# Optimization experiments

Measured on AMD Instinct MI355X. Metric: run time of the kernel, lower is better.

## Reference

```python
import jax, jax.numpy as jnp
import numpy as np

MARGIN = 0.9
WIN = 3
SIGMA = 1.5    # kornia ssim default gaussian sigma
PAD = (WIN - 1) // 2


def _gauss2d(win, sigma):
    x = np.arange(win, dtype=np.float64) - (win - 1) / 2.0
    g = np.exp(-(x ** 2) / (2.0 * sigma ** 2))
    g = g / g.sum()
    return jnp.asarray(np.outer(g, g), dtype=jnp.float32)

_KERN = _gauss2d(WIN, SIGMA)[None, None]


def _blur(z):
    # kornia filter2d: reflect padding + gaussian window, 'same' output
    zp = jnp.pad(z, ((0, 0), (0, 0), (PAD, PAD), (PAD, PAD)), mode='reflect')
    return jax.lax.conv_general_dilated(zp, _KERN.astype(z.dtype), (1, 1), 'VALID')


def setup_inputs() -> dict:
    key = jax.random.key(0)
    kernels = jax.random.normal(key, (128, 128, 3, 3), dtype=jnp.float32)
    return {"kernels": kernels}


def reference(kernels):
    C_in, C_out, h, w = kernels.shape
    flat = kernels.reshape(C_in * C_out, h, w)

    # pair indices (constants) -- replicate torch flatten/repeat_interleave order exactly
    bi, bj = np.triu_indices(C_out, k=1)          # P_per_ch pairs
    P = bi.shape[0]
    offs = np.arange(C_in) * C_out
    i_idx = (bi[:, None] + offs[None, :]).ravel() # [P, C_in] row-major flatten
    j_idx = (bj[:, None] + offs[None, :]).ravel()
    ch_id = jnp.asarray(np.repeat(np.arange(C_in), P), dtype=jnp.int32)

    # dynamic range (torch uses .item() -> detached)
    rng = jax.lax.stop_gradient(flat.max() - flat.min())
    rng = jnp.where(rng == 0, jnp.asarray(1.0, flat.dtype), rng)
    C1 = (0.01 * rng) ** 2
    C2 = (0.03 * rng) ** 2

    x = flat[i_idx][:, None]  # [P_total,1,h,w]
    y = flat[j_idx][:, None]

    mu1, mu2 = _blur(x), _blur(y)
    mu1_sq, mu2_sq, mu12 = mu1 * mu1, mu2 * mu2, mu1 * mu2
    s1 = _blur(x * x) - mu1_sq
    s2 = _blur(y * y) - mu2_sq
    s12 = _blur(x * y) - mu12
    ssim_map = ((2.0 * mu12 + C1) * (2.0 * s12 + C2)) / (
        (mu1_sq + mu2_sq + C1) * (s1 + s2 + C2))
    ssim_pair = ssim_map.mean(axis=(1, 2, 3))           # [P_total]

    hinge = jax.nn.relu(ssim_pair - MARGIN)
    pos = (hinge > 0).astype(flat.dtype)
    sums = jax.ops.segment_sum(hinge, ch_id, num_segments=C_in)
    counts = jax.ops.segment_sum(pos, ch_id, num_segments=C_in)
    layer_loss = (sums / jnp.maximum(counts, 1.0)).mean()
    return layer_loss  # total / n_layers with a single layer
```

## Files before the change

kernel.cpp:

```cpp
#include <hip/hip_runtime.h>
#include <math.h>

#define CIN   128
#define COUT  128
#define NMAPS (CIN*COUT)
#define PPC   8128
#define F32S  27
#define F64S  24
#define LCAP  (1u<<21)
#define BPC   8


__device__ inline void decode_pair(int p, int& a, int& b) {
    int a0 = (int)((255.0f - sqrtf((float)(65025 - 8 * p))) * 0.5f);
    if (a0 < 0) a0 = 0;
    if (a0 > 126) a0 = 126;
    while ((a0 + 1) * (255 - (a0 + 1)) / 2 <= p) ++a0;
    while (a0 * (255 - a0) / 2 > p) --a0;
    a = a0;
    b = a0 + 1 + (p - a0 * (255 - a0) / 2);
}

__device__ inline void blur3f(const float* X, float* O, float g0, float g1) {
    float h0 = 2.0f * g0;
    float T[9];
#pragma unroll
    for (int c = 0; c < 3; ++c) {
        float x0 = X[c], x1 = X[3 + c], x2 = X[6 + c];
        T[c]     = g1 * x0 + h0 * x1;
        T[3 + c] = g0 * (x0 + x2) + g1 * x1;
        T[6 + c] = h0 * x1 + g1 * x2;
    }
#pragma unroll
    for (int r = 0; r < 3; ++r) {
        float t0 = T[3 * r], t1 = T[3 * r + 1], t2 = T[3 * r + 2];
        O[3 * r]     = g1 * t0 + h0 * t1;
        O[3 * r + 1] = g0 * (t0 + t2) + g1 * t1;
        O[3 * r + 2] = h0 * t1 + g1 * t2;
    }
}

__device__ inline void blur3d(const double* X, double* O, double g0, double g1) {
    double h0 = 2.0 * g0;
    double T[9];
#pragma unroll
    for (int c = 0; c < 3; ++c) {
        double x0 = X[c], x1 = X[3 + c], x2 = X[6 + c];
        T[c]     = g1 * x0 + h0 * x1;
        T[3 + c] = g0 * (x0 + x2) + g1 * x1;
        T[6 + c] = h0 * x1 + g1 * x2;
    }
#pragma unroll
    for (int r = 0; r < 3; ++r) {
        double t0 = T[3 * r], t1 = T[3 * r + 1], t2 = T[3 * r + 2];
        O[3 * r]     = g1 * t0 + h0 * t1;
        O[3 * r + 1] = g0 * (t0 + t2) + g1 * t1;
        O[3 * r + 2] = h0 * t1 + g1 * t2;
    }
}


__global__ __launch_bounds__(256) void k_pre(const float* __restrict__ in,
                                             float* __restrict__ pre32,
                                             double* __restrict__ pre64,
                                             float* __restrict__ pbmin,
                                             float* __restrict__ pbmax,
                                             float* __restrict__ segsum,
                                             float* __restrict__ segcnt,
                                             unsigned* __restrict__ listc,
                                             float g0f, float g1f,
                                             double g0, double g1) {
    __shared__ float stg[2304];
    int tid = threadIdx.x;
    int base = blockIdx.x * 2304;
    for (int i = tid; i < 2304; i += 256) stg[i] = in[base + i];
    __syncthreads();

    float xf[9];
    float lmin = 1e30f, lmax = -1e30f;
#pragma unroll
    for (int k = 0; k < 9; ++k) {
        xf[k] = stg[tid * 9 + k];
        lmin = fminf(lmin, xf[k]);
        lmax = fmaxf(lmax, xf[k]);
    }
    int m = blockIdx.x * 256 + tid;

    {
        float mu[9], q[9], bq[9];
        blur3f(xf, mu, g0f, g1f);
#pragma unroll
        for (int k = 0; k < 9; ++k) q[k] = xf[k] * xf[k];
        blur3f(q, bq, g0f, g1f);
        float* o = pre32 + m * F32S;
#pragma unroll
        for (int k = 0; k < 9; ++k) {
            o[k]      = xf[k];
            o[9 + k]  = mu[k];
            o[18 + k] = bq[k] - mu[k] * mu[k];
        }
    }
    {
        double xd[9], mud[9], qd[9], bqd[9];
#pragma unroll
        for (int k = 0; k < 9; ++k) xd[k] = (double)xf[k];
        blur3d(xd, mud, g0, g1);
#pragma unroll
        for (int k = 0; k < 9; ++k) qd[k] = xd[k] * xd[k];
        blur3d(qd, bqd, g0, g1);
        double* od = pre64 + (size_t)m * F64S;
        float* odf = (float*)od;
#pragma unroll
        for (int k = 0; k < 9; ++k) odf[k] = xf[k];
#pragma unroll
        for (int k = 0; k < 9; ++k) {
            od[6 + k]  = mud[k];
            od[15 + k] = bqd[k] - mud[k] * mud[k];
        }
    }

#pragma unroll
    for (int o = 32; o > 0; o >>= 1) {
        lmin = fminf(lmin, __shfl_down(lmin, o));
        lmax = fmaxf(lmax, __shfl_down(lmax, o));
    }
    __shared__ float rmn[4], rmx[4];
    if ((tid & 63) == 0) { rmn[tid >> 6] = lmin; rmx[tid >> 6] = lmax; }
    __syncthreads();
    if (tid == 0) {
        pbmin[blockIdx.x] = fminf(fminf(rmn[0], rmn[1]), fminf(rmn[2], rmn[3]));
        pbmax[blockIdx.x] = fmaxf(fmaxf(rmx[0], rmx[1]), fmaxf(rmx[2], rmx[3]));
    }
    if (blockIdx.x == 0) {
        if (tid < 128) { segsum[tid] = 0.0f; segcnt[tid] = 0.0f; }
        if (tid == 128) *listc = 0u;
    }
}


__global__ __launch_bounds__(256) void k_pairs(const float* __restrict__ pre32,
                                               const float* __restrict__ pbmin,
                                               const float* __restrict__ pbmax,
                                               unsigned* __restrict__ listc,
                                               unsigned* __restrict__ list,
                                               double* __restrict__ c12,
                                               float g0f, float g1f) {
    __shared__ float P[COUT * F32S];
    __shared__ float cc[2];
    int tid = threadIdx.x;
    int c = blockIdx.x >> 3, q = blockIdx.x & 7;

    const float* src = pre32 + (size_t)c * COUT * F32S;
    for (int i = tid; i < COUT * F32S; i += 256) P[i] = src[i];

    if (tid < 64) {
        float mn = pbmin[tid], mx = pbmax[tid];
#pragma unroll
        for (int o = 32; o > 0; o >>= 1) {
            mn = fminf(mn, __shfl_down(mn, o));
            mx = fmaxf(mx, __shfl_down(mx, o));
        }
        if (tid == 0) {
            double rng = (double)mx - (double)mn;
            if (rng == 0.0) rng = 1.0;
            double C1 = (0.01 * rng) * (0.01 * rng);
            double C2 = (0.03 * rng) * (0.03 * rng);
            cc[0] = (float)C1; cc[1] = (float)C2;
            if (blockIdx.x == 0) { c12[0] = C1; c12[1] = C2; }
        }
    }
    __syncthreads();
    float C1 = cc[0], C2 = cc[1];

#pragma unroll
    for (int it = 0; it < 4; ++it) {
        int p = it * 2048 + q * 256 + tid;
        if (p >= PPC) break;
        int a, b;
        decode_pair(p, a, b);
        const float* A = P + a * F32S;
        const float* B = P + b * F32S;

        float z[9], bz[9];
#pragma unroll
        for (int k = 0; k < 9; ++k) z[k] = A[k] * B[k];
        blur3f(z, bz, g0f, g1f);

        float an = 0.0f, ad = 1.0f;
#pragma unroll
        for (int k = 0; k < 9; ++k) {
            float ma = A[9 + k], mb = B[9 + k];
            float mu12 = ma * mb;
            float s12  = bz[k] - mu12;
            float nn = fmaf(2.0f, mu12, C1) * fmaf(2.0f, s12, C2);
            float dd = fmaf(ma, ma, fmaf(mb, mb, C1)) * (A[18 + k] + B[18 + k] + C2);
            an = an * dd + nn * ad;
            ad *= dd;
        }
        float ssim = an / (ad * 9.0f);
        if (ssim > 0.897f) {
            unsigned idx = atomicAdd(listc, 1u);
            if (idx < LCAP) list[idx] = (unsigned)((c << 13) | p);
        }
    }
}


__global__ __launch_bounds__(256) void k_fb(const double* __restrict__ pre64,
                                            const unsigned* __restrict__ listc,
                                            const unsigned* __restrict__ list,
                                            const double* __restrict__ c12,
                                            float* __restrict__ segsum,
                                            float* __restrict__ segcnt,
                                            double g0, double g1) {
    unsigned n = *listc;
    if (n > LCAP) n = LCAP;
    double C1 = c12[0], C2 = c12[1];
    for (unsigned i = blockIdx.x * 256 + threadIdx.x; i < n; i += gridDim.x * 256) {
        unsigned u = list[i];
        int c = (int)(u >> 13), p = (int)(u & 8191);
        int a, b;
        decode_pair(p, a, b);
        const double* Pa = pre64 + ((size_t)c * COUT + a) * F64S;
        const double* Pb = pre64 + ((size_t)c * COUT + b) * F64S;
        const float* xa = (const float*)Pa;
        const float* xb = (const float*)Pb;

        double z[9], bz[9];
#pragma unroll
        for (int k = 0; k < 9; ++k) z[k] = (double)xa[k] * (double)xb[k];
        blur3d(z, bz, g0, g1);

        double ssum = 0.0;
#pragma unroll
        for (int k = 0; k < 9; ++k) {
            double ma = Pa[6 + k], mb = Pb[6 + k];
            double mu12 = ma * mb;
            double s12  = bz[k] - mu12;
            double num  = (2.0 * mu12 + C1) * (2.0 * s12 + C2);
            double den  = (ma * ma + mb * mb + C1) * (Pa[15 + k] + Pb[15 + k] + C2);
            ssum += num / den;
        }
        double hg = ssum / 9.0 - 0.9;
        if (hg > 0.0) {
            unsigned seg = (unsigned)(p * 128 + c) / 8128u;
            atomicAdd(&segsum[seg], (float)hg);
            atomicAdd(&segcnt[seg], 1.0f);
        }
    }
}


__global__ __launch_bounds__(128) void k_fin(const float* __restrict__ segsum,
                                             const float* __restrict__ segcnt,
                                             float* __restrict__ out) {
    int t = threadIdx.x;
    double v = (double)segsum[t] / fmax((double)segcnt[t], 1.0);
#pragma unroll
    for (int o = 32; o > 0; o >>= 1) v += __shfl_down(v, o);
    __shared__ double ws2[2];
    if ((t & 63) == 0) ws2[t >> 6] = v;
    __syncthreads();
    if (t == 0) out[0] = (float)((ws2[0] + ws2[1]) * (1.0 / 128.0));
}


extern "C" void kernel_launch(void* const* d_in, const int* in_sizes, int n_in,
                              void* d_out, int out_size, void* d_ws, size_t ws_size,
                              hipStream_t stream) {
    const float* in = (const float*)d_in[0];
    float* out = (float*)d_out;
    char* ws = (char*)d_ws;

    float*    pbmin  = (float*)(ws + 0);
    float*    pbmax  = (float*)(ws + 256);
    float*    segsum = (float*)(ws + 512);
    float*    segcnt = (float*)(ws + 1024);
    unsigned* listc  = (unsigned*)(ws + 1536);
    double*   c12    = (double*)(ws + 1544);
    float*    pre32  = (float*)(ws + 2048);
    double*   pre64  = (double*)(ws + 2048 + 1769472);
    unsigned* list   = (unsigned*)(ws + 2048 + 1769472 + 3145728);

    double e = exp(-1.0 / 4.5);
    double s = 2.0 * e + 1.0;
    double g0 = e / s, g1 = 1.0 / s;
    float g0f = (float)g0, g1f = (float)g1;

    k_pre  <<<NMAPS / 256, 256, 0, stream>>>(in, pre32, pre64, pbmin, pbmax,
                                             segsum, segcnt, listc, g0f, g1f, g0, g1);
    k_pairs<<<CIN * BPC, 256, 0, stream>>>(pre32, pbmin, pbmax, listc, list, c12, g0f, g1f);
    k_fb   <<<128, 256, 0, stream>>>(pre64, listc, list, c12, segsum, segcnt, g0, g1);
    k_fin  <<<1, 128, 0, stream>>>(segsum, segcnt, out);
}
```

Measured before the change: 78.79 us.

## Fuse precompute, pair screening, fp64 fallback and finalize into one kernel

Replaces the four-kernel pipeline with a small min/max kernel plus one fused kernel per channel. The fused kernel recomputes per-map blurred statistics in shared memory, screens pairs in fp32 and immediately refines candidates in fp64. Hinge sums go into block-local shared accumulators, and the last block finalizes the result through a done counter. This removes the global pre32/pre64 buffers, the candidate list and two launches. In exchange it uses only 256 blocks and puts divergent fp64 work inline in the screening loop.

```diff
diff --git a/kernel.cpp b/kernel.cpp
--- a/kernel.cpp
+++ b/kernel.cpp
@@ -3,12 +3,8 @@
 
 #define CIN   128
 #define COUT  128
-#define NMAPS (CIN*COUT)
 #define PPC   8128
-#define F32S  27
-#define F64S  24
-#define LCAP  (1u<<21)
-#define BPC   8
+#define NFLT  (CIN*COUT*9)
 
 
 __device__ inline void decode_pair(int p, int& a, int& b) {
@@ -60,65 +56,19 @@
 }
 
 
-__global__ __launch_bounds__(256) void k_pre(const float* __restrict__ in,
-                                             float* __restrict__ pre32,
-                                             double* __restrict__ pre64,
-                                             float* __restrict__ pbmin,
-                                             float* __restrict__ pbmax,
-                                             float* __restrict__ segsum,
-                                             float* __restrict__ segcnt,
-                                             unsigned* __restrict__ listc,
-                                             float g0f, float g1f,
-                                             double g0, double g1) {
-    __shared__ float stg[2304];
+__global__ __launch_bounds__(256) void k_minmax(const float* __restrict__ in,
+                                                float* __restrict__ pbmin,
+                                                float* __restrict__ pbmax,
+                                                float* __restrict__ segsum,
+                                                float* __restrict__ segcnt,
+                                                unsigned* __restrict__ done) {
     int tid = threadIdx.x;
-    int base = blockIdx.x * 2304;
-    for (int i = tid; i < 2304; i += 256) stg[i] = in[base + i];
-    __syncthreads();
-
-    float xf[9];
     float lmin = 1e30f, lmax = -1e30f;
-#pragma unroll
-    for (int k = 0; k < 9; ++k) {
-        xf[k] = stg[tid * 9 + k];
-        lmin = fminf(lmin, xf[k]);
-        lmax = fmaxf(lmax, xf[k]);
-    }
-    int m = blockIdx.x * 256 + tid;
-
-    {
-        float mu[9], q[9], bq[9];
-        blur3f(xf, mu, g0f, g1f);
-#pragma unroll
-        for (int k = 0; k < 9; ++k) q[k] = xf[k] * xf[k];
-        blur3f(q, bq, g0f, g1f);
-        float* o = pre32 + m * F32S;
-#pragma unroll
-        for (int k = 0; k < 9; ++k) {
-            o[k]      = xf[k];
-            o[9 + k]  = mu[k];
-            o[18 + k] = bq[k] - mu[k] * mu[k];
-        }
-    }
-    {
-        double xd[9], mud[9], qd[9], bqd[9];
-#pragma unroll
-        for (int k = 0; k < 9; ++k) xd[k] = (double)xf[k];
-        blur3d(xd, mud, g0, g1);
-#pragma unroll
-        for (int k = 0; k < 9; ++k) qd[k] = xd[k] * xd[k];
-        blur3d(qd, bqd, g0, g1);
-        double* od = pre64 + (size_t)m * F64S;
-        float* odf = (float*)od;
-#pragma unroll
-        for (int k = 0; k < 9; ++k) odf[k] = xf[k];
-#pragma unroll
-        for (int k = 0; k < 9; ++k) {
-            od[6 + k]  = mud[k];
-            od[15 + k] = bqd[k] - mud[k] * mud[k];
-        }
-    }
-
+    for (int i = blockIdx.x * 256 + tid; i < NFLT; i += 64 * 256) {
+        float v = in[i];
+        lmin = fminf(lmin, v);
+        lmax = fmaxf(lmax, v);
+    }
 #pragma unroll
     for (int o = 32; o > 0; o >>= 1) {
         lmin = fminf(lmin, __shfl_down(lmin, o));
@@ -132,26 +82,34 @@
         pbmax[blockIdx.x] = fmaxf(fmaxf(rmx[0], rmx[1]), fmaxf(rmx[2], rmx[3]));
     }
     if (blockIdx.x == 0) {
-        if (tid < 128) { segsum[tid] = 0.0f; segcnt[tid] = 0.0f; }
-        if (tid == 128) *listc = 0u;
-    }
-}
-
-
-__global__ __launch_bounds__(256) void k_pairs(const float* __restrict__ pre32,
-                                               const float* __restrict__ pbmin,
-                                               const float* __restrict__ pbmax,
-                                               unsigned* __restrict__ listc,
-                                               unsigned* __restrict__ list,
-                                               double* __restrict__ c12,
-                                               float g0f, float g1f) {
-    __shared__ float P[COUT * F32S];
-    __shared__ float cc[2];
+        if (tid < 128)       { segsum[tid] = 0.0f; segcnt[tid] = 0.0f; }
+        else if (tid == 128) { *done = 0u; }
+    }
+}
+
+
+__global__ __launch_bounds__(256) void k_main(const float* __restrict__ in,
+                                              const float* __restrict__ pbmin,
+                                              const float* __restrict__ pbmax,
+                                              float* __restrict__ segsum,
+                                              float* __restrict__ segcnt,
+                                              unsigned* __restrict__ done,
+                                              float* __restrict__ out,
+                                              float g0f, float g1f,
+                                              double g0, double g1) {
+    __shared__ float  s32[COUT * 27];
+    __shared__ double s64[COUT * 19];
+    __shared__ float  stg[COUT * 9];
+    __shared__ float  bs[128], bc[128];
+    __shared__ float  cf[2];
+    __shared__ double cd[2];
+    __shared__ int    lastflag;
+
     int tid = threadIdx.x;
-    int c = blockIdx.x >> 3, q = blockIdx.x & 7;
-
-    const float* src = pre32 + (size_t)c * COUT * F32S;
-    for (int i = tid; i < COUT * F32S; i += 256) P[i] = src[i];
+    int c = blockIdx.x >> 1, q = blockIdx.x & 1;
+
+    const float* src = in + c * (COUT * 9);
+    for (int i = tid; i < COUT * 9; i += 256) stg[i] = src[i];
 
     if (tid < 64) {
         float mn = pbmin[tid], mx = pbmax[tid];
@@ -165,21 +123,53 @@
             if (rng == 0.0) rng = 1.0;
             double C1 = (0.01 * rng) * (0.01 * rng);
             double C2 = (0.03 * rng) * (0.03 * rng);
-            cc[0] = (float)C1; cc[1] = (float)C2;
-            if (blockIdx.x == 0) { c12[0] = C1; c12[1] = C2; }
-        }
-    }
-    __syncthreads();
-    float C1 = cc[0], C2 = cc[1];
-
-#pragma unroll
-    for (int it = 0; it < 4; ++it) {
-        int p = it * 2048 + q * 256 + tid;
-        if (p >= PPC) break;
+            cd[0] = C1; cd[1] = C2;
+            cf[0] = (float)C1; cf[1] = (float)C2;
+        }
+    }
+    if (tid < 128) { bs[tid] = 0.0f; bc[tid] = 0.0f; }
+    __syncthreads();
+
+    if (tid < COUT) {
+        float xf[9];
+#pragma unroll
+        for (int k = 0; k < 9; ++k) xf[k] = stg[tid * 9 + k];
+        float mu[9], qq[9], bq[9];
+        blur3f(xf, mu, g0f, g1f);
+#pragma unroll
+        for (int k = 0; k < 9; ++k) qq[k] = xf[k] * xf[k];
+        blur3f(qq, bq, g0f, g1f);
+        float* o = s32 + tid * 27;
+#pragma unroll
+        for (int k = 0; k < 9; ++k) {
+            o[k]      = xf[k];
+            o[9 + k]  = mu[k];
+            o[18 + k] = bq[k] - mu[k] * mu[k];
+        }
+        double xd[9], mud[9], qd[9], bqd[9];
+#pragma unroll
+        for (int k = 0; k < 9; ++k) xd[k] = (double)xf[k];
+        blur3d(xd, mud, g0, g1);
+#pragma unroll
+        for (int k = 0; k < 9; ++k) qd[k] = xd[k] * xd[k];
+        blur3d(qd, bqd, g0, g1);
+        double* od = s64 + tid * 19;
+#pragma unroll
+        for (int k = 0; k < 9; ++k) {
+            od[k]     = mud[k];
+            od[9 + k] = bqd[k] - mud[k] * mud[k];
+        }
+    }
+    __syncthreads();
+
+    float C1 = cf[0], C2 = cf[1];
+    double C1d = cd[0], C2d = cd[1];
+
+    for (int p = tid + 256 * q; p < PPC; p += 512) {
         int a, b;
         decode_pair(p, a, b);
-        const float* A = P + a * F32S;
-        const float* B = P + b * F32S;
+        const float* A = s32 + a * 27;
+        const float* B = s32 + b * 27;
 
         float z[9], bz[9];
 #pragma unroll
@@ -198,70 +188,63 @@
             ad *= dd;
         }
         float ssim = an / (ad * 9.0f);
-        if (ssim > 0.897f) {
-            unsigned idx = atomicAdd(listc, 1u);
-            if (idx < LCAP) list[idx] = (unsigned)((c << 13) | p);
-        }
-    }
-}
-
-
-__global__ __launch_bounds__(256) void k_fb(const double* __restrict__ pre64,
-                                            const unsigned* __restrict__ listc,
-                                            const unsigned* __restrict__ list,
-                                            const double* __restrict__ c12,
-                                            float* __restrict__ segsum,
-                                            float* __restrict__ segcnt,
-                                            double g0, double g1) {
-    unsigned n = *listc;
-    if (n > LCAP) n = LCAP;
-    double C1 = c12[0], C2 = c12[1];
-    for (unsigned i = blockIdx.x * 256 + threadIdx.x; i < n; i += gridDim.x * 256) {
-        unsigned u = list[i];
-        int c = (int)(u >> 13), p = (int)(u & 8191);
-        int a, b;
-        decode_pair(p, a, b);
-        const double* Pa = pre64 + ((size_t)c * COUT + a) * F64S;
-        const double* Pb = pre64 + ((size_t)c * COUT + b) * F64S;
-        const float* xa = (const float*)Pa;
-        const float* xb = (const float*)Pb;
-
-        double z[9], bz[9];
-#pragma unroll
-        for (int k = 0; k < 9; ++k) z[k] = (double)xa[k] * (double)xb[k];
-        blur3d(z, bz, g0, g1);
-
-        double ssum = 0.0;
-#pragma unroll
-        for (int k = 0; k < 9; ++k) {
-            double ma = Pa[6 + k], mb = Pb[6 + k];
-            double mu12 = ma * mb;
-            double s12  = bz[k] - mu12;
-            double num  = (2.0 * mu12 + C1) * (2.0 * s12 + C2);
-            double den  = (ma * ma + mb * mb + C1) * (Pa[15 + k] + Pb[15 + k] + C2);
-            ssum += num / den;
-        }
-        double hg = ssum / 9.0 - 0.9;
-        if (hg > 0.0) {
-            unsigned seg = (unsigned)(p * 128 + c) / 8128u;
-            atomicAdd(&segsum[seg], (float)hg);
-            atomicAdd(&segcnt[seg], 1.0f);
-        }
-    }
-}
-
-
-__global__ __launch_bounds__(128) void k_fin(const float* __restrict__ segsum,
-                                             const float* __restrict__ segcnt,
-                                             float* __restrict__ out) {
-    int t = threadIdx.x;
-    double v = (double)segsum[t] / fmax((double)segcnt[t], 1.0);
-#pragma unroll
-    for (int o = 32; o > 0; o >>= 1) v += __shfl_down(v, o);
-    __shared__ double ws2[2];
-    if ((t & 63) == 0) ws2[t >> 6] = v;
-    __syncthreads();
-    if (t == 0) out[0] = (float)((ws2[0] + ws2[1]) * (1.0 / 128.0));
+
+        if (!(ssim <= 0.897f)) {
+            const double* MA = s64 + a * 19;
+            const double* MB = s64 + b * 19;
+            double zd[9], bzd[9];
+#pragma unroll
+            for (int k = 0; k < 9; ++k) zd[k] = (double)A[k] * (double)B[k];
+            blur3d(zd, bzd, g0, g1);
+            double ssum = 0.0;
+#pragma unroll
+            for (int k = 0; k < 9; ++k) {
+                double ma = MA[k], mb = MB[k];
+                double mu12 = ma * mb;
+                double s12  = bzd[k] - mu12;
+                double num  = (2.0 * mu12 + C1d) * (2.0 * s12 + C2d);
+                double den  = (ma * ma + mb * mb + C1d) * (MA[9 + k] + MB[9 + k] + C2d);
+                ssum += num / den;
+            }
+            double hg = ssum / 9.0 - 0.9;
+            if (hg > 0.0) {
+                unsigned seg = (unsigned)(p * 128 + c) / 8128u;
+                atomicAdd(&bs[seg], (float)hg);
+                atomicAdd(&bc[seg], 1.0f);
+            }
+        }
+    }
+    __syncthreads();
+
+    if (tid < 128) {
+        float s = bs[tid], n = bc[tid];
+        if (s != 0.0f || n != 0.0f) {
+            atomicAdd(&segsum[tid], s);
+            atomicAdd(&segcnt[tid], n);
+        }
+        __threadfence();
+    }
+    __syncthreads();
+
+    if (tid == 0) {
+        unsigned t = atomicAdd(done, 1u);
+        lastflag = (t == (unsigned)(gridDim.x - 1));
+    }
+    __syncthreads();
+    if (lastflag) {
+        double v = 0.0;
+        if (tid < 128) {
+            float s = atomicAdd(&segsum[tid], 0.0f);
+            float n = atomicAdd(&segcnt[tid], 0.0f);
+            v = (double)s / fmax((double)n, 1.0);
+        }
+#pragma unroll
+        for (int o = 32; o > 0; o >>= 1) v += __shfl_down(v, o);
+        __shared__ double w2[2];
+        if (tid < 128 && (tid & 63) == 0) w2[tid >> 6] = v;
+        __syncthreads();
+        if (tid == 0) out[0] = (float)((w2[0] + w2[1]) * (1.0 / 128.0));
+    }
 }
 
 
@@ -276,20 +259,14 @@
     float*    pbmax  = (float*)(ws + 256);
     float*    segsum = (float*)(ws + 512);
     float*    segcnt = (float*)(ws + 1024);
-    unsigned* listc  = (unsigned*)(ws + 1536);
-    double*   c12    = (double*)(ws + 1544);
-    float*    pre32  = (float*)(ws + 2048);
-    double*   pre64  = (double*)(ws + 2048 + 1769472);
-    unsigned* list   = (unsigned*)(ws + 2048 + 1769472 + 3145728);
+    unsigned* done   = (unsigned*)(ws + 1536);
 
     double e = exp(-1.0 / 4.5);
     double s = 2.0 * e + 1.0;
     double g0 = e / s, g1 = 1.0 / s;
     float g0f = (float)g0, g1f = (float)g1;
 
-    k_pre  <<<NMAPS / 256, 256, 0, stream>>>(in, pre32, pre64, pbmin, pbmax,
-                                             segsum, segcnt, listc, g0f, g1f, g0, g1);
-    k_pairs<<<CIN * BPC, 256, 0, stream>>>(pre32, pbmin, pbmax, listc, list, c12, g0f, g1f);
-    k_fb   <<<128, 256, 0, stream>>>(pre64, listc, list, c12, segsum, segcnt, g0, g1);
-    k_fin  <<<1, 128, 0, stream>>>(segsum, segcnt, out);
-}
+    k_minmax<<<64, 256, 0, stream>>>(in, pbmin, pbmax, segsum, segcnt, done);
+    k_main  <<<CIN * 2, 256, 0, stream>>>(in, pbmin, pbmax, segsum, segcnt, done, out,
+                                          g0f, g1f, g0, g1);
+}
```

Result: slower. 80.52 us (+2.2%).
